# Kernel optimization log

Measured on AMD Instinct MI355X. Metric: run time of the kernel, lower is better.

## Reference

```python
import jax, jax.numpy as jnp
import numpy as np

N_GRAPHS = 100
NODES_PER_GRAPH = 1000
N = N_GRAPHS * NODES_PER_GRAPH
DEG = 16
E = N * DEG
IN_FEATS = 64
HIDDEN = 128
READOUT_DIM = HIDDEN // 2
SLOPE = 0.01
EPS = 1e-5


def leaky(x):
    return jnp.where(x >= 0, x, SLOPE * x)


def _kaiming(k, shape):
    # torch kaiming_uniform_, fan_in mode, leaky_relu gain
    fan_in = shape[0]
    gain = np.sqrt(2.0 / (1.0 + SLOPE ** 2))
    bound = gain * np.sqrt(3.0 / fan_in)
    return jax.random.uniform(k, shape, jnp.float32, -bound, bound)


def setup_inputs() -> dict:
    key = jax.random.key(0)
    ks = jax.random.split(key, 16)
    node_feats = jax.random.normal(ks[0], (N, IN_FEATS), jnp.float32)
    # within-graph random edges (batched graph of equal-sized components)
    src_local = jax.random.randint(ks[1], (E,), 0, NODES_PER_GRAPH)
    dst_local = jax.random.randint(ks[2], (E,), 0, NODES_PER_GRAPH)
    edge_graph = jnp.repeat(jnp.arange(N_GRAPHS, dtype=jnp.int32), E // N_GRAPHS)
    src = (edge_graph * NODES_PER_GRAPH + src_local).astype(jnp.int32)
    dst = (edge_graph * NODES_PER_GRAPH + dst_local).astype(jnp.int32)
    edge_weights = jax.random.uniform(ks[3], (E,), jnp.float32)
    node_graph = jnp.repeat(jnp.arange(N_GRAPHS, dtype=jnp.int32), NODES_PER_GRAPH)
    return {
        "node_feats": node_feats,
        "edge_weights": edge_weights,
        "W1": _kaiming(ks[4], (IN_FEATS, HIDDEN)),
        "W2": _kaiming(ks[5], (HIDDEN, HIDDEN)),
        "gn1_alpha": jnp.ones((HIDDEN,), jnp.float32),
        "gn1_gamma": jnp.ones((HIDDEN,), jnp.float32),
        "gn1_beta": jnp.zeros((HIDDEN,), jnp.float32),
        "gn2_alpha": jnp.ones((HIDDEN,), jnp.float32),
        "gn2_gamma": jnp.ones((HIDDEN,), jnp.float32),
        "gn2_beta": jnp.zeros((HIDDEN,), jnp.float32),
        "r1_w1": _kaiming(ks[6], (HIDDEN, HIDDEN)),
        "r1_b1": jnp.zeros((HIDDEN,), jnp.float32),
        "r1_w2": _kaiming(ks[7], (HIDDEN, READOUT_DIM)),
        "r1_b2": jnp.zeros((READOUT_DIM,), jnp.float32),
        "r2_w1": _kaiming(ks[8], (HIDDEN, HIDDEN)),
        "r2_b1": jnp.zeros((HIDDEN,), jnp.float32),
        "r2_w2": _kaiming(ks[9], (HIDDEN, READOUT_DIM)),
        "r2_b2": jnp.zeros((READOUT_DIM,), jnp.float32),
        "src": src,
        "dst": dst,
        "node_graph": node_graph,
    }


def _graph_conv(x, W, src, dst, ew, out_isqrt, in_isqrt):
    # DGL GraphConv norm='both', no bias: D_in^{-1/2} A_w D_out^{-1/2} X W
    h = (x * out_isqrt[:, None]) @ W                 # [N, out]
    m = h[src] * ew[:, None]                         # [E, out] gather + edge weight
    agg = jax.ops.segment_sum(m, dst, num_segments=N)  # scatter-add
    return agg * in_isqrt[:, None]


def _graph_norm(x, alpha, gamma, beta, node_graph, inv_cnt):
    mean = jax.ops.segment_sum(x, node_graph, num_segments=N_GRAPHS) * inv_cnt
    sub = x - alpha * mean[node_graph]
    var = jax.ops.segment_sum(sub * sub, node_graph, num_segments=N_GRAPHS) * inv_cnt
    return gamma * sub / jnp.sqrt(var[node_graph] + EPS) + beta


def _readout(x, w1, b1, w2, b2, node_graph, inv_cnt):
    # deep-sets style universal readout: rho(mean(phi(h_v)))
    h = leaky(x @ w1 + b1)
    pooled = jax.ops.segment_sum(h, node_graph, num_segments=N_GRAPHS) * inv_cnt
    return leaky(pooled @ w2 + b2)


def reference(node_feats, edge_weights, W1, W2,
              gn1_alpha, gn1_gamma, gn1_beta,
              gn2_alpha, gn2_gamma, gn2_beta,
              r1_w1, r1_b1, r1_w2, r1_b2,
              r2_w1, r2_b1, r2_w2, r2_b2,
              src, dst, node_graph):
    ones_e = jnp.ones((E,), jnp.float32)
    out_deg = jnp.clip(jax.ops.segment_sum(ones_e, src, num_segments=N), 1.0)
    in_deg = jnp.clip(jax.ops.segment_sum(ones_e, dst, num_segments=N), 1.0)
    out_isqrt = jax.lax.rsqrt(out_deg)
    in_isqrt = jax.lax.rsqrt(in_deg)
    inv_cnt = 1.0 / NODES_PER_GRAPH

    h = _graph_conv(node_feats, W1, src, dst, edge_weights, out_isqrt, in_isqrt)
    h = leaky(_graph_norm(h, gn1_alpha, gn1_gamma, gn1_beta, node_graph, inv_cnt))
    # dropout is identity in eval mode
    r1 = _readout(h, r1_w1, r1_b1, r1_w2, r1_b2, node_graph, inv_cnt)
    m1 = jax.ops.segment_sum(h, node_graph, num_segments=N_GRAPHS) * inv_cnt

    h = _graph_conv(h, W2, src, dst, edge_weights, out_isqrt, in_isqrt)
    h = leaky(_graph_norm(h, gn2_alpha, gn2_gamma, gn2_beta, node_graph, inv_cnt))
    r2 = _readout(h, r2_w1, r2_b1, r2_w2, r2_b2, node_graph, inv_cnt)
    m2 = jax.ops.segment_sum(h, node_graph, num_segments=N_GRAPHS) * inv_cnt

    readout = jnp.concatenate([r1, m1, r2, m2], axis=1)  # [G, 2*H + 2*H/2] = [100, 384]
    return leaky(readout)
```

## Files before the change

### kernel.cpp

```cpp
#include <hip/hip_runtime.h>
#include <cstddef>
#include <cstdint>

#define NG   100
#define NPG  1000
#define NN   (NG * NPG)
#define NE   (NN * 16)
#define EPG  (NE / NG)
#define CSRG 40000
#define MINREC 20
#define FIN  64
#define HID  128
#define RD   64
#define SLOPE 0.01f
#define EPSV  1e-5f
#define NSTRIP 250
#define GSN   40

using short8 = __attribute__((ext_vector_type(8))) short;
using f32x4  = __attribute__((ext_vector_type(4))) float;
typedef unsigned short u16;

__device__ __forceinline__ float leaky(float x) { return x >= 0.f ? x : SLOPE * x; }

__device__ __forceinline__ u16 f2bf(float f) {
  union { float f; unsigned u; } v; v.f = f;
  return (u16)((v.u + 0x7fffu + ((v.u >> 16) & 1u)) >> 16);
}
__device__ __forceinline__ float bf2f(u16 u) {
  union { unsigned u; float f; } v; v.u = ((unsigned)u) << 16;
  return v.f;
}

__device__ __forceinline__ bool swz(int b, int per_g, int& g, int& part) {
  const int xcd = b & 7;
  const int slot = b >> 3;
  g = xcd + 8 * (slot / per_g);
  part = slot % per_g;
  return g < NG;
}

__global__ __launch_bounds__(256) void wt_k(const float* __restrict__ W1,
                                            const float* __restrict__ W2,
                                            const float* __restrict__ R1,
                                            const float* __restrict__ R2,
                                            u16* __restrict__ Wt1,
                                            u16* __restrict__ Wt2,
                                            u16* __restrict__ Rt1,
                                            u16* __restrict__ Rt2) {
  const int idx = blockIdx.x * 256 + threadIdx.x;
  if (idx < FIN * HID) {
    const int n = idx >> 6, k = idx & 63;
    Wt1[idx] = f2bf(W1[k * HID + n]);
  } else {
    const int j = idx - FIN * HID;
    const int m = j >> 14, r = j & 16383;
    const int n = r >> 7, k = r & 127;
    const float* s = (m == 0) ? W2 : (m == 1) ? R1 : R2;
    u16* d = (m == 0) ? Wt2 : (m == 1) ? Rt1 : Rt2;
    d[r] = f2bf(s[k * HID + n]);
  }
}

__global__ __launch_bounds__(1024) void build_k(const int* __restrict__ src,
                                                const int* __restrict__ dst,
                                                const float* __restrict__ ew,
                                                int* __restrict__ cin_,
                                                int* __restrict__ cout_,
                                                int* __restrict__ offs,
                                                unsigned* __restrict__ csr) {
  __shared__ int hin[NPG];
  __shared__ int hout[NPG];
  __shared__ int cur[NPG];
  __shared__ int wtot[16];
  int g, part;
  if (!swz(blockIdx.x, 1, g, part)) return;
  const int t = threadIdx.x;
  const int lane = t & 63, wave = t >> 6;
  const int nb = g * NPG, eb = g * EPG;
  if (t < NPG) { hin[t] = 0; hout[t] = 0; }
  __syncthreads();
  for (int e = t; e < EPG; e += 4096) {
    int s4[4], d4[4];
#pragma unroll
    for (int k = 0; k < 4; ++k) {
      const int ee = e + k * 1024;
      if (ee < EPG) { s4[k] = src[eb + ee]; d4[k] = dst[eb + ee]; }
      else d4[k] = -1;
    }
#pragma unroll
    for (int k = 0; k < 4; ++k)
      if (d4[k] >= 0) {
        atomicAdd(&hout[s4[k] - nb], 1);
        atomicAdd(&hin[d4[k] - nb], 1);
      }
  }
  __syncthreads();
  int v[4], vr[4];
  int loc = 0;
#pragma unroll
  for (int k = 0; k < 4; ++k) {
    const int idx = t * 4 + k;
    v[k] = (idx < NPG) ? hin[idx] : 0;
    const int c4 = (v[k] + 3) & ~3;
    vr[k] = (idx < NPG) ? ((c4 > MINREC) ? c4 : MINREC) : 0;
    loc += vr[k];
  }
  int incl = loc;
#pragma unroll
  for (int d = 1; d < 64; d <<= 1) {
    const int x = __shfl_up(incl, d);
    if (lane >= d) incl += x;
  }
  if (lane == 63) wtot[wave] = incl;
  if (t < NPG) { cin_[nb + t] = hin[t]; cout_[nb + t] = hout[t]; }
  __syncthreads();
  int wexc = 0;
  for (int i = 0; i < wave; ++i) wexc += wtot[i];
  int run = g * CSRG + wexc + (incl - loc);
#pragma unroll
  for (int k = 0; k < 4; ++k) {
    const int idx = t * 4 + k;
    if (idx < NPG) {
      offs[nb + idx] = run;
      cur[idx] = run;
      for (int z = v[k]; z < vr[k]; ++z) csr[run + z] = 0;
      run += vr[k];
    }
  }
  __syncthreads();
  for (int e = t; e < EPG; e += 4096) {
    int s4[4], d4[4]; float w4[4];
#pragma unroll
    for (int k = 0; k < 4; ++k) {
      const int ee = e + k * 1024;
      if (ee < EPG) { s4[k] = src[eb + ee]; d4[k] = dst[eb + ee]; w4[k] = ew[eb + ee]; }
      else d4[k] = -1;
    }
#pragma unroll
    for (int k = 0; k < 4; ++k)
      if (d4[k] >= 0) {
        const int pos = atomicAdd(&cur[d4[k] - nb], 1);
        csr[pos] = ((unsigned)(s4[k] - nb) << 16) | (unsigned)f2bf(w4[k]);
      }
  }
}

__global__ __launch_bounds__(256) void gemm1_k(const float* __restrict__ X,
                                               const u16* __restrict__ Wt,
                                               const int* __restrict__ cout_,
                                               u16* __restrict__ Y) {
  __shared__ u16 Xl[64 * FIN];
  __shared__ u16 Wl[HID * FIN];
  const int tid = threadIdx.x;
  const int wave = tid >> 6, lane = tid & 63, l15 = lane & 15, quad = lane >> 4;
  int g, part;
  if (!swz(blockIdx.x, 4, g, part)) return;
  const int base = g * NPG + part * NSTRIP;
  const int kq = tid & 15;
  const int srow = tid >> 4;

  for (int i = tid; i < HID * (FIN / 8); i += 256) {
    const int n = i >> 3, c = i & 7;
    const short8 w = *(const short8*)(Wt + n * FIN + c * 8);
    *(short8*)&Wl[n * FIN + ((c ^ (n & 7)) << 3)] = w;
  }
  float4 xpre[4];
#pragma unroll
  for (int it = 0; it < 4; ++it) {
    const int rowi = srow + it * 16;
    xpre[it] = (rowi < NSTRIP) ? *(const float4*)(X + (size_t)(base + rowi) * FIN + kq * 4)
                               : make_float4(0.f, 0.f, 0.f, 0.f);
  }
  for (int pass = 0; pass < 4; ++pass) {
    __syncthreads();
#pragma unroll
    for (int it = 0; it < 4; ++it) {
      const int r = srow + it * 16;
      ushort4 u = make_ushort4(f2bf(xpre[it].x), f2bf(xpre[it].y),
                               f2bf(xpre[it].z), f2bf(xpre[it].w));
      const int c = kq >> 1, half = kq & 1;
      *(ushort4*)&Xl[r * FIN + (((c ^ (r & 7)) << 3) | (half << 2))] = u;
    }
    __syncthreads();
    if (pass < 3) {
#pragma unroll
      for (int it = 0; it < 4; ++it) {
        const int rowi = (pass + 1) * 64 + srow + it * 16;
        xpre[it] = (rowi < NSTRIP) ? *(const float4*)(X + (size_t)(base + rowi) * FIN + kq * 4)
                                   : make_float4(0.f, 0.f, 0.f, 0.f);
      }
    }
    short8 a[2];
    const int arow = wave * 16 + l15;
#pragma unroll
    for (int kt = 0; kt < 2; ++kt)
      a[kt] = *(const short8*)&Xl[arow * FIN + (((kt * 4 + quad) ^ (l15 & 7)) << 3)];
    float sc[4];
    int rows[4];
#pragma unroll
    for (int r = 0; r < 4; ++r) {
      rows[r] = pass * 64 + wave * 16 + quad * 4 + r;
      sc[r] = (rows[r] < NSTRIP) ? rsqrtf(fmaxf((float)cout_[base + rows[r]], 1.0f)) : 0.f;
    }
#pragma unroll
    for (int ct = 0; ct < 8; ++ct) {
      f32x4 acc = {0.f, 0.f, 0.f, 0.f};
      const int brow = ct * 16 + l15;
#pragma unroll
      for (int kt = 0; kt < 2; ++kt) {
        const short8 b = *(const short8*)&Wl[brow * FIN + (((kt * 4 + quad) ^ (l15 & 7)) << 3)];
        acc = __builtin_amdgcn_mfma_f32_16x16x32_bf16(a[kt], b, acc, 0, 0, 0);
      }
      const int n = ct * 16 + l15;
#pragma unroll
      for (int r = 0; r < 4; ++r)
        if (rows[r] < NSTRIP) Y[(size_t)(base + rows[r]) * HID + n] = f2bf(acc[r] * sc[r]);
    }
  }
}

__device__ __forceinline__ void norm_affine(const float* sx, const float* sq,
                                            const float* alpha, const float* gamma,
                                            const float* beta, int g, int c8,
                                            float* Av, float* Bv) {
  const float inv = 1.0f / NPG;
#pragma unroll
  for (int j = 0; j < 8; ++j) {
    const int f = c8 * 8 + j;
    const float mean = sx[g * HID + f] * inv;
    const float ex2 = sq[g * HID + f] * inv;
    const float am = alpha[f] * mean;
    const float var = fmaxf(ex2 - 2.0f * am * mean + am * am, 0.0f);
    const float A = gamma[f] * rsqrtf(var + EPSV);
    Av[j] = A;
    Bv[j] = beta[f] - A * am;
  }
}

__global__ __launch_bounds__(256) void gemm_norm_k(const u16* __restrict__ Xb,
                                                   const u16* __restrict__ Wt,
                                                   const float* __restrict__ sx,
                                                   const float* __restrict__ sq,
                                                   const float* __restrict__ alpha,
                                                   const float* __restrict__ gamma,
                                                   const float* __restrict__ beta,
                                                   const int* __restrict__ cout_,
                                                   u16* __restrict__ Y) {
  __shared__ u16 Xl[64 * HID];
  __shared__ u16 Wl[HID * HID];
  const int tid = threadIdx.x;
  const int wave = tid >> 6, lane = tid & 63, l15 = lane & 15, quad = lane >> 4;
  int g, part;
  if (!swz(blockIdx.x, 4, g, part)) return;
  const int base = g * NPG + part * NSTRIP;
  const int c8 = tid & 15;
  const int srow = tid >> 4;

  for (int i = tid; i < HID * (HID / 8); i += 256) {
    const int n = i >> 4, c = i & 15;
    const short8 w = *(const short8*)(Wt + n * HID + c * 8);
    *(short8*)&Wl[n * HID + ((c ^ (n & 15)) << 3)] = w;
  }
  float Av[8], Bv[8];
  norm_affine(sx, sq, alpha, gamma, beta, g, c8, Av, Bv);
  const short8 z8 = {0, 0, 0, 0, 0, 0, 0, 0};
  short8 xpre[4];
#pragma unroll
  for (int it = 0; it < 4; ++it) {
    const int rowi = srow + it * 16;
    xpre[it] = (rowi < NSTRIP) ? *(const short8*)(Xb + (size_t)(base + rowi) * HID + c8 * 8) : z8;
  }
  for (int pass = 0; pass < 4; ++pass) {
    __syncthreads();
#pragma unroll
    for (int it = 0; it < 4; ++it) {
      const int r = srow + it * 16;
      const int rowi = pass * 64 + r;
      short8 o = z8;
      if (rowi < NSTRIP) {
#pragma unroll
        for (int j = 0; j < 8; ++j)
          o[j] = (short)f2bf(leaky(fmaf(Av[j], bf2f((u16)xpre[it][j]), Bv[j])));
      }
      *(short8*)&Xl[r * HID + ((c8 ^ (r & 15)) << 3)] = o;
    }
    __syncthreads();
    if (pass < 3) {
#pragma unroll
      for (int it = 0; it < 4; ++it) {
        const int rowi = (pass + 1) * 64 + srow + it * 16;
        xpre[it] = (rowi < NSTRIP) ? *(const short8*)(Xb + (size_t)(base + rowi) * HID + c8 * 8) : z8;
      }
    }
    short8 a[4];
    const int arow = wave * 16 + l15;
#pragma unroll
    for (int kt = 0; kt < 4; ++kt)
      a[kt] = *(const short8*)&Xl[arow * HID + (((kt * 4 + quad) ^ l15) << 3)];
    float sc[4];
    int rows[4];
#pragma unroll
    for (int r = 0; r < 4; ++r) {
      rows[r] = pass * 64 + wave * 16 + quad * 4 + r;
      sc[r] = (rows[r] < NSTRIP) ? rsqrtf(fmaxf((float)cout_[base + rows[r]], 1.0f)) : 0.f;
    }
#pragma unroll
    for (int ct = 0; ct < 8; ++ct) {
      f32x4 acc = {0.f, 0.f, 0.f, 0.f};
      const int brow = ct * 16 + l15;
#pragma unroll
      for (int kt = 0; kt < 4; ++kt) {
        const short8 b = *(const short8*)&Wl[brow * HID + (((kt * 4 + quad) ^ l15) << 3)];
        acc = __builtin_amdgcn_mfma_f32_16x16x32_bf16(a[kt], b, acc, 0, 0, 0);
      }
      const int n = ct * 16 + l15;
#pragma unroll
      for (int r = 0; r < 4; ++r)
        if (rows[r] < NSTRIP) Y[(size_t)(base + rows[r]) * HID + n] = f2bf(acc[r] * sc[r]);
    }
  }
}

struct RedT { float red[16][HID]; float hred[16][HID]; };
union ShT { u16 Xl[64 * HID]; RedT r; };

__global__ __launch_bounds__(256) void phi_pool_k(const u16* __restrict__ Xb,
                                                  const float* __restrict__ sx,
                                                  const float* __restrict__ sq,
                                                  const float* __restrict__ alpha,
                                                  const float* __restrict__ gamma,
                                                  const float* __restrict__ beta,
                                                  const u16* __restrict__ Wt,
                                                  const float* __restrict__ b1,
                                                  float* __restrict__ phi_sum,
                                                  float* __restrict__ h_sum) {
  __shared__ ShT sh;
  __shared__ u16 Wl[HID * HID];
  const int tid = threadIdx.x;
  const int wave = tid >> 6, lane = tid & 63, l15 = lane & 15, quad = lane >> 4;
  int g, part;
  if (!swz(blockIdx.x, 4, g, part)) return;
  const int base = g * NPG + part * NSTRIP;
  const int c8 = tid & 15;
  const int srow = tid >> 4;

  for (int i = tid; i < HID * (HID / 8); i += 256) {
    const int n = i >> 4, c = i & 15;
    const short8 w = *(const short8*)(Wt + n * HID + c * 8);
    *(short8*)&Wl[n * HID + ((c ^ (n & 15)) << 3)] = w;
  }
  float Av[8], Bv[8];
  norm_affine(sx, sq, alpha, gamma, beta, g, c8, Av, Bv);
  float bcol[8];
#pragma unroll
  for (int ct = 0; ct < 8; ++ct) bcol[ct] = b1[ct * 16 + l15];

  float pooled[8] = {0.f, 0.f, 0.f, 0.f, 0.f, 0.f, 0.f, 0.f};
  float hp[8] = {0.f, 0.f, 0.f, 0.f, 0.f, 0.f, 0.f, 0.f};
  const short8 z8 = {0, 0, 0, 0, 0, 0, 0, 0};
  short8 xpre[4];
#pragma unroll
  for (int it = 0; it < 4; ++it) {
    const int rowi = srow + it * 16;
    xpre[it] = (rowi < NSTRIP) ? *(const short8*)(Xb + (size_t)(base + rowi) * HID + c8 * 8) : z8;
  }
  for (int pass = 0; pass < 4; ++pass) {
    __syncthreads();
#pragma unroll
    for (int it = 0; it < 4; ++it) {
      const int r = srow + it * 16;
      const int rowi = pass * 64 + r;
      short8 o = z8;
      if (rowi < NSTRIP) {
#pragma unroll
        for (int j = 0; j < 8; ++j) {
          const float xn = leaky(fmaf(Av[j], bf2f((u16)xpre[it][j]), Bv[j]));
          hp[j] += xn;
          o[j] = (short)f2bf(xn);
        }
      }
      *(short8*)&sh.Xl[r * HID + ((c8 ^ (r & 15)) << 3)] = o;
    }
    __syncthreads();
    if (pass < 3) {
#pragma unroll
      for (int it = 0; it < 4; ++it) {
        const int rowi = (pass + 1) * 64 + srow + it * 16;
        xpre[it] = (rowi < NSTRIP) ? *(const short8*)(Xb + (size_t)(base + rowi) * HID + c8 * 8) : z8;
      }
    }
    short8 a[4];
    const int arow = wave * 16 + l15;
#pragma unroll
    for (int kt = 0; kt < 4; ++kt)
      a[kt] = *(const short8*)&sh.Xl[arow * HID + (((kt * 4 + quad) ^ l15) << 3)];
#pragma unroll
    for (int ct = 0; ct < 8; ++ct) {
      f32x4 acc = {0.f, 0.f, 0.f, 0.f};
      const int brow = ct * 16 + l15;
#pragma unroll
      for (int kt = 0; kt < 4; ++kt) {
        const short8 b = *(const short8*)&Wl[brow * HID + (((kt * 4 + quad) ^ l15) << 3)];
        acc = __builtin_amdgcn_mfma_f32_16x16x32_bf16(a[kt], b, acc, 0, 0, 0);
      }
#pragma unroll
      for (int r = 0; r < 4; ++r) {
        const int rowi = pass * 64 + wave * 16 + quad * 4 + r;
        if (rowi < NSTRIP) pooled[ct] += leaky(acc[r] + bcol[ct]);
      }
    }
  }
  __syncthreads();
  const int qi = wave * 4 + quad;
#pragma unroll
  for (int ct = 0; ct < 8; ++ct) sh.r.red[qi][ct * 16 + l15] = pooled[ct];
#pragma unroll
  for (int j = 0; j < 8; ++j) sh.r.hred[tid >> 4][(tid & 15) * 8 + j] = hp[j];
  __syncthreads();
  if (tid < HID) {
    float s = 0.f;
#pragma unroll
    for (int q = 0; q < 16; ++q) s += sh.r.red[q][tid];
    unsafeAtomicAdd(&phi_sum[g * HID + tid], s);
  } else {
    const int t = tid - HID;
    float s = 0.f;
#pragma unroll
    for (int rr = 0; rr < 16; ++rr) s += sh.r.hred[rr][t];
    unsafeAtomicAdd(&h_sum[g * HID + t], s);
  }
}

__global__ __launch_bounds__(256) void gather_k(const u16* __restrict__ H,
                                                const unsigned* __restrict__ csr,
                                                const int* __restrict__ offs,
                                                const int* __restrict__ cin_,
                                                u16* __restrict__ AGG,
                                                float* __restrict__ sx,
                                                float* __restrict__ sq) {
  __shared__ float redx[4][HID];
  __shared__ float redq[4][HID];
  const int wave = threadIdx.x >> 6;
  const int lane = threadIdx.x & 63;
  int g, part;
  if (!swz(blockIdx.x, 25, g, part)) return;
  const int nb = g * NPG;
  const int base = nb + part * GSN;
  const int loff = lane * 2;
  const u16* __restrict__ Hg = H + (size_t)nb * HID;

  float sxa = 0.f, sxb = 0.f, sqa = 0.f, sqb = 0.f;
  for (int it = 0; it < 3; ++it) {
    const int nc = (it < 2) ? 4 : 2;
    int nn[4], off[4], cnt[4], c4p[4];
    float isq[4];
    const uint4* p[4];
#pragma unroll
    for (int c = 0; c < 4; ++c) {
      const int j = it * 4 + c;
      const int node = base + wave + ((j < 10) ? j : 0) * 4;
      nn[c] = node;
      const int nu = __builtin_amdgcn_readfirstlane(node);
      off[c] = __builtin_amdgcn_readfirstlane(offs[nu]);
      cnt[c] = (c < nc) ? __builtin_amdgcn_readfirstlane(cin_[nu]) : 0;
      const int cr = (cnt[c] + 3) & ~3;
      c4p[c] = ((cr > MINREC) ? cr : MINREC) >> 2;
      isq[c] = rsqrtf(fmaxf((float)cnt[c], 1.0f));
      p[c] = (const uint4*)__builtin_assume_aligned(csr + off[c], 16);
    }
    float ax[4] = {0.f, 0.f, 0.f, 0.f};
    float ay[4] = {0.f, 0.f, 0.f, 0.f};
#pragma unroll
    for (int t = 0; t < 5; ++t) {
      uint4 r[4];
      unsigned u[4][4];
#pragma unroll
      for (int c = 0; c < 4; ++c)
        if (c < nc) {
          r[c] = p[c][t];
          u[c][0] = *(const unsigned*)(Hg + (size_t)(r[c].x >> 16) * HID + loff);
          u[c][1] = *(const unsigned*)(Hg + (size_t)(r[c].y >> 16) * HID + loff);
          u[c][2] = *(const unsigned*)(Hg + (size_t)(r[c].z >> 16) * HID + loff);
          u[c][3] = *(const unsigned*)(Hg + (size_t)(r[c].w >> 16) * HID + loff);
        }
#pragma unroll
      for (int c = 0; c < 4; ++c)
        if (c < nc) {
          const float w0 = bf2f((u16)(r[c].x & 0xffffu));
          const float w1 = bf2f((u16)(r[c].y & 0xffffu));
          const float w2 = bf2f((u16)(r[c].z & 0xffffu));
          const float w3 = bf2f((u16)(r[c].w & 0xffffu));
          ax[c] = fmaf(w0, __uint_as_float(u[c][0] << 16), ax[c]);
          ay[c] = fmaf(w0, __uint_as_float(u[c][0] & 0xffff0000u), ay[c]);
          ax[c] = fmaf(w1, __uint_as_float(u[c][1] << 16), ax[c]);
          ay[c] = fmaf(w1, __uint_as_float(u[c][1] & 0xffff0000u), ay[c]);
          ax[c] = fmaf(w2, __uint_as_float(u[c][2] << 16), ax[c]);
          ay[c] = fmaf(w2, __uint_as_float(u[c][2] & 0xffff0000u), ay[c]);
          ax[c] = fmaf(w3, __uint_as_float(u[c][3] << 16), ax[c]);
          ay[c] = fmaf(w3, __uint_as_float(u[c][3] & 0xffff0000u), ay[c]);
        }
    }
#pragma unroll
    for (int c = 0; c < 4; ++c) {
      for (int t = 5; t < c4p[c]; ++t) {
        const uint4 r = p[c][t];
        const unsigned u0 = *(const unsigned*)(Hg + (size_t)(r.x >> 16) * HID + loff);
        const unsigned u1 = *(const unsigned*)(Hg + (size_t)(r.y >> 16) * HID + loff);
        const unsigned u2 = *(const unsigned*)(Hg + (size_t)(r.z >> 16) * HID + loff);
        const unsigned u3 = *(const unsigned*)(Hg + (size_t)(r.w >> 16) * HID + loff);
        const float w0 = bf2f((u16)(r.x & 0xffffu));
        const float w1 = bf2f((u16)(r.y & 0xffffu));
        const float w2 = bf2f((u16)(r.z & 0xffffu));
        const float w3 = bf2f((u16)(r.w & 0xffffu));
        ax[c] = fmaf(w0, __uint_as_float(u0 << 16), ax[c]);
        ay[c] = fmaf(w0, __uint_as_float(u0 & 0xffff0000u), ay[c]);
        ax[c] = fmaf(w1, __uint_as_float(u1 << 16), ax[c]);
        ay[c] = fmaf(w1, __uint_as_float(u1 & 0xffff0000u), ay[c]);
        ax[c] = fmaf(w2, __uint_as_float(u2 << 16), ax[c]);
        ay[c] = fmaf(w2, __uint_as_float(u2 & 0xffff0000u), ay[c]);
        ax[c] = fmaf(w3, __uint_as_float(u3 << 16), ax[c]);
        ay[c] = fmaf(w3, __uint_as_float(u3 & 0xffff0000u), ay[c]);
      }
    }
#pragma unroll
    for (int c = 0; c < 4; ++c)
      if (c < nc) {
        const float rx = ax[c] * isq[c];
        const float ry = ay[c] * isq[c];
        *(unsigned*)(AGG + (size_t)nn[c] * HID + loff) =
            (unsigned)f2bf(rx) | ((unsigned)f2bf(ry) << 16);
        sxa += rx; sxb += ry;
        sqa += rx * rx; sqb += ry * ry;
      }
  }
  redx[wave][loff] = sxa; redx[wave][loff + 1] = sxb;
  redq[wave][loff] = sqa; redq[wave][loff + 1] = sqb;
  __syncthreads();
  const int tid = threadIdx.x;
  if (tid < HID) {
    unsafeAtomicAdd(&sx[g * HID + tid],
                    redx[0][tid] + redx[1][tid] + redx[2][tid] + redx[3][tid]);
  } else {
    const int t = tid - HID;
    unsafeAtomicAdd(&sq[g * HID + t],
                    redq[0][t] + redq[1][t] + redq[2][t] + redq[3][t]);
  }
}

__global__ __launch_bounds__(64) void finalize_k(const float* __restrict__ phi_sum,
                                                 const float* __restrict__ h_sum,
                                                 const float* __restrict__ w2,
                                                 const float* __restrict__ b2,
                                                 float* __restrict__ out,
                                                 int roff, int moff) {
  const int g = blockIdx.x;
  const int j = threadIdx.x;
  float acc = b2[j];
#pragma unroll 8
  for (int k = 0; k < HID; ++k)
    acc += (phi_sum[g * HID + k] * (1.0f / NPG)) * w2[k * RD + j];
  const float r = leaky(acc);
  out[g * 384 + roff + j] = leaky(r);
  out[g * 384 + moff + j] = leaky(h_sum[g * HID + j] * (1.0f / NPG));
  out[g * 384 + moff + 64 + j] = leaky(h_sum[g * HID + 64 + j] * (1.0f / NPG));
}

extern "C" void kernel_launch(void* const* d_in, const int* in_sizes, int n_in,
                              void* d_out, int out_size, void* d_ws, size_t ws_size,
                              hipStream_t stream) {
  const float* node_feats = (const float*)d_in[0];
  const float* ew   = (const float*)d_in[1];
  const float* W1   = (const float*)d_in[2];
  const float* W2   = (const float*)d_in[3];
  const float* g1a  = (const float*)d_in[4];
  const float* g1g  = (const float*)d_in[5];
  const float* g1b  = (const float*)d_in[6];
  const float* g2a  = (const float*)d_in[7];
  const float* g2g  = (const float*)d_in[8];
  const float* g2b  = (const float*)d_in[9];
  const float* r1w1 = (const float*)d_in[10];
  const float* r1b1 = (const float*)d_in[11];
  const float* r1w2 = (const float*)d_in[12];
  const float* r1b2 = (const float*)d_in[13];
  const float* r2w1 = (const float*)d_in[14];
  const float* r2b1 = (const float*)d_in[15];
  const float* r2w2 = (const float*)d_in[16];
  const float* r2b2 = (const float*)d_in[17];
  const int* src = (const int*)d_in[18];
  const int* dst = (const int*)d_in[19];
  float* out = (float*)d_out;

  char* wsb = (char*)d_ws;
  float* ps1     = (float*)wsb;
  float* hs1     = ps1 + NG * HID;
  float* ps2     = hs1 + NG * HID;
  float* hs2     = ps2 + NG * HID;
  float* sx1     = hs2 + NG * HID;
  float* sq1     = sx1 + NG * HID;
  float* sx2     = sq1 + NG * HID;
  float* sq2     = sx2 + NG * HID;
  int*   cin     = (int*)(sq2 + NG * HID);
  int*   cout_   = cin + NN;
  int*   offs    = cout_ + NN;
  unsigned* csr  = (unsigned*)(offs + NN);
  u16*   Wt1     = (u16*)(csr + (size_t)NG * CSRG);
  u16*   Wt2     = Wt1 + HID * FIN;
  u16*   Rt1     = Wt2 + HID * HID;
  u16*   Rt2     = Rt1 + HID * HID;
  u16*   bufA    = Rt2 + HID * HID;
  u16*   bufB    = bufA + (size_t)NN * HID;

  hipMemsetAsync(d_ws, 0, (size_t)(8 * NG * HID) * sizeof(float), stream);

  wt_k<<<(FIN * HID + 3 * HID * HID) / 256, 256, 0, stream>>>(
      W1, W2, r1w1, r2w1, Wt1, Wt2, Rt1, Rt2);
  build_k<<<8 * 13, 1024, 0, stream>>>(src, dst, ew, cin, cout_, offs, csr);

  const int gemm_grid = 8 * 4 * 13;
  const int gather_grid = 8 * 25 * 13;

  gemm1_k<<<gemm_grid, 256, 0, stream>>>(node_feats, Wt1, cout_, bufA);
  gather_k<<<gather_grid, 256, 0, stream>>>(bufA, csr, offs, cin, bufB, sx1, sq1);
  phi_pool_k<<<gemm_grid, 256, 0, stream>>>(bufB, sx1, sq1, g1a, g1g, g1b,
                                            Rt1, r1b1, ps1, hs1);
  finalize_k<<<NG, 64, 0, stream>>>(ps1, hs1, r1w2, r1b2, out, 0, 64);

  gemm_norm_k<<<gemm_grid, 256, 0, stream>>>(bufB, Wt2, sx1, sq1, g1a, g1g, g1b,
                                             cout_, bufA);
  gather_k<<<gather_grid, 256, 0, stream>>>(bufA, csr, offs, cin, bufB, sx2, sq2);
  phi_pool_k<<<gemm_grid, 256, 0, stream>>>(bufB, sx2, sq2, g2a, g2g, g2b,
                                            Rt2, r2b1, ps2, hs2);
  finalize_k<<<NG, 64, 0, stream>>>(ps2, hs2, r2w2, r2b2, out, 192, 256);
}
```

Measured before the change: 294.2 us.

## Fuse all per-graph stages into one persistent 1024-thread block per graph

```diff
diff --git a/kernel.cpp b/kernel.cpp
--- a/kernel.cpp
+++ b/kernel.cpp
@@ -14,8 +14,6 @@
 #define RD   64
 #define SLOPE 0.01f
 #define EPSV  1e-5f
-#define NSTRIP 250
-#define GSN   40
 
 using short8 = __attribute__((ext_vector_type(8))) short;
 using f32x4  = __attribute__((ext_vector_type(4))) float;
@@ -30,14 +28,6 @@
 __device__ __forceinline__ float bf2f(u16 u) {
   union { unsigned u; float f; } v; v.u = ((unsigned)u) << 16;
   return v.f;
-}
-
-__device__ __forceinline__ bool swz(int b, int per_g, int& g, int& part) {
-  const int xcd = b & 7;
-  const int slot = b >> 3;
-  g = xcd + 8 * (slot / per_g);
-  part = slot % per_g;
-  return g < NG;
 }
 
 __global__ __launch_bounds__(256) void wt_k(const float* __restrict__ W1,
@@ -62,449 +52,73 @@
   }
 }
 
-__global__ __launch_bounds__(1024) void build_k(const int* __restrict__ src,
-                                                const int* __restrict__ dst,
-                                                const float* __restrict__ ew,
-                                                int* __restrict__ cin_,
-                                                int* __restrict__ cout_,
-                                                int* __restrict__ offs,
-                                                unsigned* __restrict__ csr) {
-  __shared__ int hin[NPG];
-  __shared__ int hout[NPG];
-  __shared__ int cur[NPG];
-  __shared__ int wtot[16];
-  int g, part;
-  if (!swz(blockIdx.x, 1, g, part)) return;
+struct BldU { int cur[NPG]; int wtot[16]; };
+struct RedU { float redx[16][HID]; float redq[16][HID]; };
+struct PhiU { float red4[4][HID]; float hred[16][HID]; };
+union MegaU { BldU b; u16 Xl[64 * HID]; RedU r; PhiU p; };
+
+__device__ __forceinline__ void gather_stage(const u16* __restrict__ Hg,
+                                             const unsigned* __restrict__ csr,
+                                             u16* __restrict__ AGGg, MegaU* u,
+                                             const int* s_hin, const int* s_offs,
+                                             float* s_sx, float* s_sq) {
   const int t = threadIdx.x;
-  const int lane = t & 63, wave = t >> 6;
-  const int nb = g * NPG, eb = g * EPG;
-  if (t < NPG) { hin[t] = 0; hout[t] = 0; }
-  __syncthreads();
-  for (int e = t; e < EPG; e += 4096) {
-    int s4[4], d4[4];
-#pragma unroll
-    for (int k = 0; k < 4; ++k) {
-      const int ee = e + k * 1024;
-      if (ee < EPG) { s4[k] = src[eb + ee]; d4[k] = dst[eb + ee]; }
-      else d4[k] = -1;
-    }
-#pragma unroll
-    for (int k = 0; k < 4; ++k)
-      if (d4[k] >= 0) {
-        atomicAdd(&hout[s4[k] - nb], 1);
-        atomicAdd(&hin[d4[k] - nb], 1);
-      }
-  }
-  __syncthreads();
-  int v[4], vr[4];
-  int loc = 0;
-#pragma unroll
-  for (int k = 0; k < 4; ++k) {
-    const int idx = t * 4 + k;
-    v[k] = (idx < NPG) ? hin[idx] : 0;
-    const int c4 = (v[k] + 3) & ~3;
-    vr[k] = (idx < NPG) ? ((c4 > MINREC) ? c4 : MINREC) : 0;
-    loc += vr[k];
-  }
-  int incl = loc;
-#pragma unroll
-  for (int d = 1; d < 64; d <<= 1) {
-    const int x = __shfl_up(incl, d);
-    if (lane >= d) incl += x;
-  }
-  if (lane == 63) wtot[wave] = incl;
-  if (t < NPG) { cin_[nb + t] = hin[t]; cout_[nb + t] = hout[t]; }
-  __syncthreads();
-  int wexc = 0;
-  for (int i = 0; i < wave; ++i) wexc += wtot[i];
-  int run = g * CSRG + wexc + (incl - loc);
-#pragma unroll
-  for (int k = 0; k < 4; ++k) {
-    const int idx = t * 4 + k;
-    if (idx < NPG) {
-      offs[nb + idx] = run;
-      cur[idx] = run;
-      for (int z = v[k]; z < vr[k]; ++z) csr[run + z] = 0;
-      run += vr[k];
-    }
-  }
-  __syncthreads();
-  for (int e = t; e < EPG; e += 4096) {
-    int s4[4], d4[4]; float w4[4];
-#pragma unroll
-    for (int k = 0; k < 4; ++k) {
-      const int ee = e + k * 1024;
-      if (ee < EPG) { s4[k] = src[eb + ee]; d4[k] = dst[eb + ee]; w4[k] = ew[eb + ee]; }
-      else d4[k] = -1;
-    }
-#pragma unroll
-    for (int k = 0; k < 4; ++k)
-      if (d4[k] >= 0) {
-        const int pos = atomicAdd(&cur[d4[k] - nb], 1);
-        csr[pos] = ((unsigned)(s4[k] - nb) << 16) | (unsigned)f2bf(w4[k]);
-      }
-  }
-}
-
-__global__ __launch_bounds__(256) void gemm1_k(const float* __restrict__ X,
-                                               const u16* __restrict__ Wt,
-                                               const int* __restrict__ cout_,
-                                               u16* __restrict__ Y) {
-  __shared__ u16 Xl[64 * FIN];
-  __shared__ u16 Wl[HID * FIN];
-  const int tid = threadIdx.x;
-  const int wave = tid >> 6, lane = tid & 63, l15 = lane & 15, quad = lane >> 4;
-  int g, part;
-  if (!swz(blockIdx.x, 4, g, part)) return;
-  const int base = g * NPG + part * NSTRIP;
-  const int kq = tid & 15;
-  const int srow = tid >> 4;
-
-  for (int i = tid; i < HID * (FIN / 8); i += 256) {
-    const int n = i >> 3, c = i & 7;
-    const short8 w = *(const short8*)(Wt + n * FIN + c * 8);
-    *(short8*)&Wl[n * FIN + ((c ^ (n & 7)) << 3)] = w;
-  }
-  float4 xpre[4];
-#pragma unroll
-  for (int it = 0; it < 4; ++it) {
-    const int rowi = srow + it * 16;
-    xpre[it] = (rowi < NSTRIP) ? *(const float4*)(X + (size_t)(base + rowi) * FIN + kq * 4)
-                               : make_float4(0.f, 0.f, 0.f, 0.f);
-  }
-  for (int pass = 0; pass < 4; ++pass) {
-    __syncthreads();
-#pragma unroll
-    for (int it = 0; it < 4; ++it) {
-      const int r = srow + it * 16;
-      ushort4 u = make_ushort4(f2bf(xpre[it].x), f2bf(xpre[it].y),
-                               f2bf(xpre[it].z), f2bf(xpre[it].w));
-      const int c = kq >> 1, half = kq & 1;
-      *(ushort4*)&Xl[r * FIN + (((c ^ (r & 7)) << 3) | (half << 2))] = u;
-    }
-    __syncthreads();
-    if (pass < 3) {
-#pragma unroll
-      for (int it = 0; it < 4; ++it) {
-        const int rowi = (pass + 1) * 64 + srow + it * 16;
-        xpre[it] = (rowi < NSTRIP) ? *(const float4*)(X + (size_t)(base + rowi) * FIN + kq * 4)
-                                   : make_float4(0.f, 0.f, 0.f, 0.f);
-      }
-    }
-    short8 a[2];
-    const int arow = wave * 16 + l15;
-#pragma unroll
-    for (int kt = 0; kt < 2; ++kt)
-      a[kt] = *(const short8*)&Xl[arow * FIN + (((kt * 4 + quad) ^ (l15 & 7)) << 3)];
-    float sc[4];
-    int rows[4];
-#pragma unroll
-    for (int r = 0; r < 4; ++r) {
-      rows[r] = pass * 64 + wave * 16 + quad * 4 + r;
-      sc[r] = (rows[r] < NSTRIP) ? rsqrtf(fmaxf((float)cout_[base + rows[r]], 1.0f)) : 0.f;
-    }
-#pragma unroll
-    for (int ct = 0; ct < 8; ++ct) {
-      f32x4 acc = {0.f, 0.f, 0.f, 0.f};
-      const int brow = ct * 16 + l15;
-#pragma unroll
-      for (int kt = 0; kt < 2; ++kt) {
-        const short8 b = *(const short8*)&Wl[brow * FIN + (((kt * 4 + quad) ^ (l15 & 7)) << 3)];
-        acc = __builtin_amdgcn_mfma_f32_16x16x32_bf16(a[kt], b, acc, 0, 0, 0);
-      }
-      const int n = ct * 16 + l15;
-#pragma unroll
-      for (int r = 0; r < 4; ++r)
-        if (rows[r] < NSTRIP) Y[(size_t)(base + rows[r]) * HID + n] = f2bf(acc[r] * sc[r]);
-    }
-  }
-}
-
-__device__ __forceinline__ void norm_affine(const float* sx, const float* sq,
-                                            const float* alpha, const float* gamma,
-                                            const float* beta, int g, int c8,
-                                            float* Av, float* Bv) {
-  const float inv = 1.0f / NPG;
-#pragma unroll
-  for (int j = 0; j < 8; ++j) {
-    const int f = c8 * 8 + j;
-    const float mean = sx[g * HID + f] * inv;
-    const float ex2 = sq[g * HID + f] * inv;
-    const float am = alpha[f] * mean;
-    const float var = fmaxf(ex2 - 2.0f * am * mean + am * am, 0.0f);
-    const float A = gamma[f] * rsqrtf(var + EPSV);
-    Av[j] = A;
-    Bv[j] = beta[f] - A * am;
-  }
-}
-
-__global__ __launch_bounds__(256) void gemm_norm_k(const u16* __restrict__ Xb,
-                                                   const u16* __restrict__ Wt,
-                                                   const float* __restrict__ sx,
-                                                   const float* __restrict__ sq,
-                                                   const float* __restrict__ alpha,
-                                                   const float* __restrict__ gamma,
-                                                   const float* __restrict__ beta,
-                                                   const int* __restrict__ cout_,
-                                                   u16* __restrict__ Y) {
-  __shared__ u16 Xl[64 * HID];
-  __shared__ u16 Wl[HID * HID];
-  const int tid = threadIdx.x;
-  const int wave = tid >> 6, lane = tid & 63, l15 = lane & 15, quad = lane >> 4;
-  int g, part;
-  if (!swz(blockIdx.x, 4, g, part)) return;
-  const int base = g * NPG + part * NSTRIP;
-  const int c8 = tid & 15;
-  const int srow = tid >> 4;
-
-  for (int i = tid; i < HID * (HID / 8); i += 256) {
-    const int n = i >> 4, c = i & 15;
-    const short8 w = *(const short8*)(Wt + n * HID + c * 8);
-    *(short8*)&Wl[n * HID + ((c ^ (n & 15)) << 3)] = w;
-  }
-  float Av[8], Bv[8];
-  norm_affine(sx, sq, alpha, gamma, beta, g, c8, Av, Bv);
-  const short8 z8 = {0, 0, 0, 0, 0, 0, 0, 0};
-  short8 xpre[4];
-#pragma unroll
-  for (int it = 0; it < 4; ++it) {
-    const int rowi = srow + it * 16;
-    xpre[it] = (rowi < NSTRIP) ? *(const short8*)(Xb + (size_t)(base + rowi) * HID + c8 * 8) : z8;
-  }
-  for (int pass = 0; pass < 4; ++pass) {
-    __syncthreads();
-#pragma unroll
-    for (int it = 0; it < 4; ++it) {
-      const int r = srow + it * 16;
-      const int rowi = pass * 64 + r;
-      short8 o = z8;
-      if (rowi < NSTRIP) {
-#pragma unroll
-        for (int j = 0; j < 8; ++j)
-          o[j] = (short)f2bf(leaky(fmaf(Av[j], bf2f((u16)xpre[it][j]), Bv[j])));
-      }
-      *(short8*)&Xl[r * HID + ((c8 ^ (r & 15)) << 3)] = o;
-    }
-    __syncthreads();
-    if (pass < 3) {
-#pragma unroll
-      for (int it = 0; it < 4; ++it) {
-        const int rowi = (pass + 1) * 64 + srow + it * 16;
-        xpre[it] = (rowi < NSTRIP) ? *(const short8*)(Xb + (size_t)(base + rowi) * HID + c8 * 8) : z8;
-      }
-    }
-    short8 a[4];
-    const int arow = wave * 16 + l15;
-#pragma unroll
-    for (int kt = 0; kt < 4; ++kt)
-      a[kt] = *(const short8*)&Xl[arow * HID + (((kt * 4 + quad) ^ l15) << 3)];
-    float sc[4];
-    int rows[4];
-#pragma unroll
-    for (int r = 0; r < 4; ++r) {
-      rows[r] = pass * 64 + wave * 16 + quad * 4 + r;
-      sc[r] = (rows[r] < NSTRIP) ? rsqrtf(fmaxf((float)cout_[base + rows[r]], 1.0f)) : 0.f;
-    }
-#pragma unroll
-    for (int ct = 0; ct < 8; ++ct) {
-      f32x4 acc = {0.f, 0.f, 0.f, 0.f};
-      const int brow = ct * 16 + l15;
-#pragma unroll
-      for (int kt = 0; kt < 4; ++kt) {
-        const short8 b = *(const short8*)&Wl[brow * HID + (((kt * 4 + quad) ^ l15) << 3)];
-        acc = __builtin_amdgcn_mfma_f32_16x16x32_bf16(a[kt], b, acc, 0, 0, 0);
-      }
-      const int n = ct * 16 + l15;
-#pragma unroll
-      for (int r = 0; r < 4; ++r)
-        if (rows[r] < NSTRIP) Y[(size_t)(base + rows[r]) * HID + n] = f2bf(acc[r] * sc[r]);
-    }
-  }
-}
-
-struct RedT { float red[16][HID]; float hred[16][HID]; };
-union ShT { u16 Xl[64 * HID]; RedT r; };
-
-__global__ __launch_bounds__(256) void phi_pool_k(const u16* __restrict__ Xb,
-                                                  const float* __restrict__ sx,
-                                                  const float* __restrict__ sq,
-                                                  const float* __restrict__ alpha,
-                                                  const float* __restrict__ gamma,
-                                                  const float* __restrict__ beta,
-                                                  const u16* __restrict__ Wt,
-                                                  const float* __restrict__ b1,
-                                                  float* __restrict__ phi_sum,
-                                                  float* __restrict__ h_sum) {
-  __shared__ ShT sh;
-  __shared__ u16 Wl[HID * HID];
-  const int tid = threadIdx.x;
-  const int wave = tid >> 6, lane = tid & 63, l15 = lane & 15, quad = lane >> 4;
-  int g, part;
-  if (!swz(blockIdx.x, 4, g, part)) return;
-  const int base = g * NPG + part * NSTRIP;
-  const int c8 = tid & 15;
-  const int srow = tid >> 4;
-
-  for (int i = tid; i < HID * (HID / 8); i += 256) {
-    const int n = i >> 4, c = i & 15;
-    const short8 w = *(const short8*)(Wt + n * HID + c * 8);
-    *(short8*)&Wl[n * HID + ((c ^ (n & 15)) << 3)] = w;
-  }
-  float Av[8], Bv[8];
-  norm_affine(sx, sq, alpha, gamma, beta, g, c8, Av, Bv);
-  float bcol[8];
-#pragma unroll
-  for (int ct = 0; ct < 8; ++ct) bcol[ct] = b1[ct * 16 + l15];
-
-  float pooled[8] = {0.f, 0.f, 0.f, 0.f, 0.f, 0.f, 0.f, 0.f};
-  float hp[8] = {0.f, 0.f, 0.f, 0.f, 0.f, 0.f, 0.f, 0.f};
-  const short8 z8 = {0, 0, 0, 0, 0, 0, 0, 0};
-  short8 xpre[4];
-#pragma unroll
-  for (int it = 0; it < 4; ++it) {
-    const int rowi = srow + it * 16;
-    xpre[it] = (rowi < NSTRIP) ? *(const short8*)(Xb + (size_t)(base + rowi) * HID + c8 * 8) : z8;
-  }
-  for (int pass = 0; pass < 4; ++pass) {
-    __syncthreads();
-#pragma unroll
-    for (int it = 0; it < 4; ++it) {
-      const int r = srow + it * 16;
-      const int rowi = pass * 64 + r;
-      short8 o = z8;
-      if (rowi < NSTRIP) {
-#pragma unroll
-        for (int j = 0; j < 8; ++j) {
-          const float xn = leaky(fmaf(Av[j], bf2f((u16)xpre[it][j]), Bv[j]));
-          hp[j] += xn;
-          o[j] = (short)f2bf(xn);
-        }
-      }
-      *(short8*)&sh.Xl[r * HID + ((c8 ^ (r & 15)) << 3)] = o;
-    }
-    __syncthreads();
-    if (pass < 3) {
-#pragma unroll
-      for (int it = 0; it < 4; ++it) {
-        const int rowi = (pass + 1) * 64 + srow + it * 16;
-        xpre[it] = (rowi < NSTRIP) ? *(const short8*)(Xb + (size_t)(base + rowi) * HID + c8 * 8) : z8;
-      }
-    }
-    short8 a[4];
-    const int arow = wave * 16 + l15;
-#pragma unroll
-    for (int kt = 0; kt < 4; ++kt)
-      a[kt] = *(const short8*)&sh.Xl[arow * HID + (((kt * 4 + quad) ^ l15) << 3)];
-#pragma unroll
-    for (int ct = 0; ct < 8; ++ct) {
-      f32x4 acc = {0.f, 0.f, 0.f, 0.f};
-      const int brow = ct * 16 + l15;
-#pragma unroll
-      for (int kt = 0; kt < 4; ++kt) {
-        const short8 b = *(const short8*)&Wl[brow * HID + (((kt * 4 + quad) ^ l15) << 3)];
-        acc = __builtin_amdgcn_mfma_f32_16x16x32_bf16(a[kt], b, acc, 0, 0, 0);
-      }
-#pragma unroll
-      for (int r = 0; r < 4; ++r) {
-        const int rowi = pass * 64 + wave * 16 + quad * 4 + r;
-        if (rowi < NSTRIP) pooled[ct] += leaky(acc[r] + bcol[ct]);
-      }
-    }
-  }
-  __syncthreads();
-  const int qi = wave * 4 + quad;
-#pragma unroll
-  for (int ct = 0; ct < 8; ++ct) sh.r.red[qi][ct * 16 + l15] = pooled[ct];
-#pragma unroll
-  for (int j = 0; j < 8; ++j) sh.r.hred[tid >> 4][(tid & 15) * 8 + j] = hp[j];
-  __syncthreads();
-  if (tid < HID) {
-    float s = 0.f;
-#pragma unroll
-    for (int q = 0; q < 16; ++q) s += sh.r.red[q][tid];
-    unsafeAtomicAdd(&phi_sum[g * HID + tid], s);
-  } else {
-    const int t = tid - HID;
-    float s = 0.f;
-#pragma unroll
-    for (int rr = 0; rr < 16; ++rr) s += sh.r.hred[rr][t];
-    unsafeAtomicAdd(&h_sum[g * HID + t], s);
-  }
-}
-
-__global__ __launch_bounds__(256) void gather_k(const u16* __restrict__ H,
-                                                const unsigned* __restrict__ csr,
-                                                const int* __restrict__ offs,
-                                                const int* __restrict__ cin_,
-                                                u16* __restrict__ AGG,
-                                                float* __restrict__ sx,
-                                                float* __restrict__ sq) {
-  __shared__ float redx[4][HID];
-  __shared__ float redq[4][HID];
-  const int wave = threadIdx.x >> 6;
-  const int lane = threadIdx.x & 63;
-  int g, part;
-  if (!swz(blockIdx.x, 25, g, part)) return;
-  const int nb = g * NPG;
-  const int base = nb + part * GSN;
+  const int wave = t >> 6, lane = t & 63;
   const int loff = lane * 2;
-  const u16* __restrict__ Hg = H + (size_t)nb * HID;
-
   float sxa = 0.f, sxb = 0.f, sqa = 0.f, sqb = 0.f;
-  for (int it = 0; it < 3; ++it) {
-    const int nc = (it < 2) ? 4 : 2;
-    int nn[4], off[4], cnt[4], c4p[4];
+  for (int it = 0; it < 16; ++it) {
+    int nn[4], cnt[4], c4p[4], val[4];
     float isq[4];
     const uint4* p[4];
 #pragma unroll
     for (int c = 0; c < 4; ++c) {
-      const int j = it * 4 + c;
-      const int node = base + wave + ((j < 10) ? j : 0) * 4;
-      nn[c] = node;
-      const int nu = __builtin_amdgcn_readfirstlane(node);
-      off[c] = __builtin_amdgcn_readfirstlane(offs[nu]);
-      cnt[c] = (c < nc) ? __builtin_amdgcn_readfirstlane(cin_[nu]) : 0;
+      const int idx = wave + 16 * (it * 4 + c);
+      val[c] = (idx < NPG);
+      const int idc = val[c] ? idx : 0;
+      nn[c] = idc;
+      const int off = __builtin_amdgcn_readfirstlane(s_offs[idc]);
+      cnt[c] = val[c] ? __builtin_amdgcn_readfirstlane(s_hin[idc]) : 0;
       const int cr = (cnt[c] + 3) & ~3;
       c4p[c] = ((cr > MINREC) ? cr : MINREC) >> 2;
       isq[c] = rsqrtf(fmaxf((float)cnt[c], 1.0f));
-      p[c] = (const uint4*)__builtin_assume_aligned(csr + off[c], 16);
+      p[c] = (const uint4*)__builtin_assume_aligned(csr + off, 16);
     }
     float ax[4] = {0.f, 0.f, 0.f, 0.f};
     float ay[4] = {0.f, 0.f, 0.f, 0.f};
 #pragma unroll
-    for (int t = 0; t < 5; ++t) {
+    for (int tt = 0; tt < 5; ++tt) {
       uint4 r[4];
-      unsigned u[4][4];
+      unsigned uu[4][4];
 #pragma unroll
       for (int c = 0; c < 4; ++c)
-        if (c < nc) {
-          r[c] = p[c][t];
-          u[c][0] = *(const unsigned*)(Hg + (size_t)(r[c].x >> 16) * HID + loff);
-          u[c][1] = *(const unsigned*)(Hg + (size_t)(r[c].y >> 16) * HID + loff);
-          u[c][2] = *(const unsigned*)(Hg + (size_t)(r[c].z >> 16) * HID + loff);
-          u[c][3] = *(const unsigned*)(Hg + (size_t)(r[c].w >> 16) * HID + loff);
+        if (val[c]) {
+          r[c] = p[c][tt];
+          uu[c][0] = *(const unsigned*)(Hg + (size_t)(r[c].x >> 16) * HID + loff);
+          uu[c][1] = *(const unsigned*)(Hg + (size_t)(r[c].y >> 16) * HID + loff);
+          uu[c][2] = *(const unsigned*)(Hg + (size_t)(r[c].z >> 16) * HID + loff);
+          uu[c][3] = *(const unsigned*)(Hg + (size_t)(r[c].w >> 16) * HID + loff);
         }
 #pragma unroll
       for (int c = 0; c < 4; ++c)
-        if (c < nc) {
+        if (val[c]) {
           const float w0 = bf2f((u16)(r[c].x & 0xffffu));
           const float w1 = bf2f((u16)(r[c].y & 0xffffu));
           const float w2 = bf2f((u16)(r[c].z & 0xffffu));
           const float w3 = bf2f((u16)(r[c].w & 0xffffu));
-          ax[c] = fmaf(w0, __uint_as_float(u[c][0] << 16), ax[c]);
-          ay[c] = fmaf(w0, __uint_as_float(u[c][0] & 0xffff0000u), ay[c]);
-          ax[c] = fmaf(w1, __uint_as_float(u[c][1] << 16), ax[c]);
-          ay[c] = fmaf(w1, __uint_as_float(u[c][1] & 0xffff0000u), ay[c]);
-          ax[c] = fmaf(w2, __uint_as_float(u[c][2] << 16), ax[c]);
-          ay[c] = fmaf(w2, __uint_as_float(u[c][2] & 0xffff0000u), ay[c]);
-          ax[c] = fmaf(w3, __uint_as_float(u[c][3] << 16), ax[c]);
-          ay[c] = fmaf(w3, __uint_as_float(u[c][3] & 0xffff0000u), ay[c]);
+          ax[c] = fmaf(w0, __uint_as_float(uu[c][0] << 16), ax[c]);
+          ay[c] = fmaf(w0, __uint_as_float(uu[c][0] & 0xffff0000u), ay[c]);
+          ax[c] = fmaf(w1, __uint_as_float(uu[c][1] << 16), ax[c]);
+          ay[c] = fmaf(w1, __uint_as_float(uu[c][1] & 0xffff0000u), ay[c]);
+          ax[c] = fmaf(w2, __uint_as_float(uu[c][2] << 16), ax[c]);
+          ay[c] = fmaf(w2, __uint_as_float(uu[c][2] & 0xffff0000u), ay[c]);
+          ax[c] = fmaf(w3, __uint_as_float(uu[c][3] << 16), ax[c]);
+          ay[c] = fmaf(w3, __uint_as_float(uu[c][3] & 0xffff0000u), ay[c]);
         }
     }
 #pragma unroll
     for (int c = 0; c < 4; ++c) {
-      for (int t = 5; t < c4p[c]; ++t) {
-        const uint4 r = p[c][t];
+      for (int tt = 5; tt < c4p[c]; ++tt) {
+        const uint4 r = p[c][tt];
         const unsigned u0 = *(const unsigned*)(Hg + (size_t)(r.x >> 16) * HID + loff);
         const unsigned u1 = *(const unsigned*)(Hg + (size_t)(r.y >> 16) * HID + loff);
         const unsigned u2 = *(const unsigned*)(Hg + (size_t)(r.z >> 16) * HID + loff);
@@ -525,45 +139,363 @@
     }
 #pragma unroll
     for (int c = 0; c < 4; ++c)
-      if (c < nc) {
+      if (val[c]) {
         const float rx = ax[c] * isq[c];
         const float ry = ay[c] * isq[c];
-        *(unsigned*)(AGG + (size_t)nn[c] * HID + loff) =
+        *(unsigned*)(AGGg + (size_t)nn[c] * HID + loff) =
             (unsigned)f2bf(rx) | ((unsigned)f2bf(ry) << 16);
         sxa += rx; sxb += ry;
         sqa += rx * rx; sqb += ry * ry;
       }
   }
-  redx[wave][loff] = sxa; redx[wave][loff + 1] = sxb;
-  redq[wave][loff] = sqa; redq[wave][loff + 1] = sqb;
-  __syncthreads();
-  const int tid = threadIdx.x;
-  if (tid < HID) {
-    unsafeAtomicAdd(&sx[g * HID + tid],
-                    redx[0][tid] + redx[1][tid] + redx[2][tid] + redx[3][tid]);
-  } else {
-    const int t = tid - HID;
-    unsafeAtomicAdd(&sq[g * HID + t],
-                    redq[0][t] + redq[1][t] + redq[2][t] + redq[3][t]);
-  }
-}
-
-__global__ __launch_bounds__(64) void finalize_k(const float* __restrict__ phi_sum,
-                                                 const float* __restrict__ h_sum,
-                                                 const float* __restrict__ w2,
-                                                 const float* __restrict__ b2,
-                                                 float* __restrict__ out,
-                                                 int roff, int moff) {
+  u->r.redx[wave][loff] = sxa; u->r.redx[wave][loff + 1] = sxb;
+  u->r.redq[wave][loff] = sqa; u->r.redq[wave][loff + 1] = sqb;
+  __syncthreads();
+  if (t < HID) {
+    float s = 0.f;
+#pragma unroll
+    for (int w = 0; w < 16; ++w) s += u->r.redx[w][t];
+    s_sx[t] = s;
+  } else if (t < 2 * HID) {
+    const int c = t - HID;
+    float s = 0.f;
+#pragma unroll
+    for (int w = 0; w < 16; ++w) s += u->r.redq[w][c];
+    s_sq[c] = s;
+  }
+  __syncthreads();
+}
+
+template <bool DO_GEMM>
+__device__ __forceinline__ void phi_stage(const u16* __restrict__ Xin,
+                                          u16* __restrict__ Yout,
+                                          const u16* __restrict__ WtG,
+                                          const u16* __restrict__ RtG,
+                                          const float* __restrict__ bias1,
+                                          const float* __restrict__ alpha,
+                                          const float* __restrict__ gamma,
+                                          const float* __restrict__ beta,
+                                          MegaU* u, u16* sW, u16* sR,
+                                          const int* s_hout,
+                                          const float* s_sx, const float* s_sq,
+                                          float* ps_out, float* hs_out) {
+  const int t = threadIdx.x;
+  const int wave = t >> 6, lane = t & 63, l15 = lane & 15, quad = lane >> 4;
+  const int rg = wave >> 2, cg = wave & 3;
+  const int c8 = t & 15, srow = t >> 4;
+
+  for (int i = t; i < HID * (HID / 8); i += 1024) {
+    const int n = i >> 4, c = i & 15;
+    if (DO_GEMM) {
+      const short8 w = *(const short8*)(WtG + n * HID + c * 8);
+      *(short8*)&sW[n * HID + ((c ^ (n & 15)) << 3)] = w;
+    }
+    const short8 w2 = *(const short8*)(RtG + n * HID + c * 8);
+    *(short8*)&sR[n * HID + ((c ^ (n & 15)) << 3)] = w2;
+  }
+  const float inv = 1.0f / NPG;
+  float Av[8], Bv[8];
+#pragma unroll
+  for (int j = 0; j < 8; ++j) {
+    const int f = c8 * 8 + j;
+    const float mean = s_sx[f] * inv;
+    const float ex2 = s_sq[f] * inv;
+    const float am = alpha[f] * mean;
+    const float var = fmaxf(ex2 - 2.0f * am * mean + am * am, 0.0f);
+    const float A = gamma[f] * rsqrtf(var + EPSV);
+    Av[j] = A;
+    Bv[j] = beta[f] - A * am;
+  }
+  float bcol[2];
+#pragma unroll
+  for (int q2 = 0; q2 < 2; ++q2) bcol[q2] = bias1[(cg * 2 + q2) * 16 + l15];
+
+  float pooled[2] = {0.f, 0.f};
+  float hp[8] = {0.f, 0.f, 0.f, 0.f, 0.f, 0.f, 0.f, 0.f};
+  const short8 z8 = {0, 0, 0, 0, 0, 0, 0, 0};
+  short8 xpre = (srow < NPG) ? *(const short8*)(Xin + (size_t)srow * HID + c8 * 8) : z8;
+
+  for (int pass = 0; pass < 16; ++pass) {
+    __syncthreads();
+    {
+      const int rowi = pass * 64 + srow;
+      short8 o = z8;
+      if (rowi < NPG) {
+#pragma unroll
+        for (int j = 0; j < 8; ++j) {
+          const float xn = leaky(fmaf(Av[j], bf2f((u16)xpre[j]), Bv[j]));
+          hp[j] += xn;
+          o[j] = (short)f2bf(xn);
+        }
+      }
+      *(short8*)&u->Xl[srow * HID + ((c8 ^ (srow & 15)) << 3)] = o;
+    }
+    __syncthreads();
+    if (pass < 15) {
+      const int rowi = (pass + 1) * 64 + srow;
+      xpre = (rowi < NPG) ? *(const short8*)(Xin + (size_t)rowi * HID + c8 * 8) : z8;
+    }
+    short8 a[4];
+    const int arow = rg * 16 + l15;
+#pragma unroll
+    for (int kt = 0; kt < 4; ++kt)
+      a[kt] = *(const short8*)&u->Xl[arow * HID + (((kt * 4 + quad) ^ l15) << 3)];
+    int rows[4];
+    float sc[4];
+#pragma unroll
+    for (int r = 0; r < 4; ++r) {
+      rows[r] = pass * 64 + rg * 16 + quad * 4 + r;
+      sc[r] = (rows[r] < NPG) ? rsqrtf(fmaxf((float)s_hout[rows[r]], 1.0f)) : 0.f;
+    }
+#pragma unroll
+    for (int q2 = 0; q2 < 2; ++q2) {
+      const int ct = cg * 2 + q2;
+      const int brow = ct * 16 + l15;
+      if (DO_GEMM) {
+        f32x4 accW = {0.f, 0.f, 0.f, 0.f};
+#pragma unroll
+        for (int kt = 0; kt < 4; ++kt) {
+          const short8 b = *(const short8*)&sW[brow * HID + (((kt * 4 + quad) ^ l15) << 3)];
+          accW = __builtin_amdgcn_mfma_f32_16x16x32_bf16(a[kt], b, accW, 0, 0, 0);
+        }
+#pragma unroll
+        for (int r = 0; r < 4; ++r)
+          if (rows[r] < NPG)
+            Yout[(size_t)rows[r] * HID + ct * 16 + l15] = f2bf(accW[r] * sc[r]);
+      }
+      f32x4 accR = {0.f, 0.f, 0.f, 0.f};
+#pragma unroll
+      for (int kt = 0; kt < 4; ++kt) {
+        const short8 b = *(const short8*)&sR[brow * HID + (((kt * 4 + quad) ^ l15) << 3)];
+        accR = __builtin_amdgcn_mfma_f32_16x16x32_bf16(a[kt], b, accR, 0, 0, 0);
+      }
+#pragma unroll
+      for (int r = 0; r < 4; ++r)
+        if (rows[r] < NPG) pooled[q2] += leaky(accR[r] + bcol[q2]);
+    }
+  }
+  __syncthreads();
+#pragma unroll
+  for (int q2 = 0; q2 < 2; ++q2) {
+    pooled[q2] += __shfl_xor(pooled[q2], 16);
+    pooled[q2] += __shfl_xor(pooled[q2], 32);
+  }
+  if (quad == 0) {
+#pragma unroll
+    for (int q2 = 0; q2 < 2; ++q2)
+      u->p.red4[rg][(cg * 2 + q2) * 16 + l15] = pooled[q2];
+  }
+#pragma unroll
+  for (int j = 0; j < 8; ++j) {
+    hp[j] += __shfl_xor(hp[j], 16);
+    hp[j] += __shfl_xor(hp[j], 32);
+  }
+  if (lane < 16) {
+#pragma unroll
+    for (int j = 0; j < 8; ++j) u->p.hred[wave][(lane & 15) * 8 + j] = hp[j];
+  }
+  __syncthreads();
+  if (t < HID) {
+    float s = 0.f;
+#pragma unroll
+    for (int k = 0; k < 4; ++k) s += u->p.red4[k][t];
+    ps_out[t] = s;
+  } else if (t < 2 * HID) {
+    const int c = t - HID;
+    float s = 0.f;
+#pragma unroll
+    for (int w = 0; w < 16; ++w) s += u->p.hred[w][c];
+    hs_out[c] = s;
+  }
+  __syncthreads();
+}
+
+__global__ __launch_bounds__(1024, 1) void mega_k(
+    const float* __restrict__ X0, const float* __restrict__ ew,
+    const int* __restrict__ src, const int* __restrict__ dst,
+    const u16* __restrict__ Wt1, const u16* __restrict__ Wt2,
+    const u16* __restrict__ Rt1, const u16* __restrict__ Rt2,
+    const float* __restrict__ g1a, const float* __restrict__ g1g,
+    const float* __restrict__ g1b, const float* __restrict__ g2a,
+    const float* __restrict__ g2g, const float* __restrict__ g2b,
+    const float* __restrict__ r1b1, const float* __restrict__ r1w2,
+    const float* __restrict__ r1b2, const float* __restrict__ r2b1,
+    const float* __restrict__ r2w2, const float* __restrict__ r2b2,
+    unsigned* __restrict__ csr, u16* __restrict__ bufA, u16* __restrict__ bufB,
+    float* __restrict__ out) {
+  __shared__ u16 sW[HID * HID];
+  __shared__ u16 sR[HID * HID];
+  __shared__ int s_hin[NPG];
+  __shared__ int s_hout[NPG];
+  __shared__ int s_offs[NPG];
+  __shared__ float s_sx[HID], s_sq[HID];
+  __shared__ float s_ps[2][HID], s_hs[2][HID];
+  __shared__ MegaU u;
+
   const int g = blockIdx.x;
-  const int j = threadIdx.x;
-  float acc = b2[j];
+  const int t = threadIdx.x;
+  const int wave = t >> 6, lane = t & 63, l15 = lane & 15, quad = lane >> 4;
+  const int nb = g * NPG, eb = g * EPG;
+
+  if (t < NPG) { s_hin[t] = 0; s_hout[t] = 0; }
+  __syncthreads();
+  for (int e = t; e < EPG; e += 4096) {
+    int s4[4], d4[4];
+#pragma unroll
+    for (int k = 0; k < 4; ++k) {
+      const int ee = e + k * 1024;
+      if (ee < EPG) { s4[k] = src[eb + ee]; d4[k] = dst[eb + ee]; }
+      else d4[k] = -1;
+    }
+#pragma unroll
+    for (int k = 0; k < 4; ++k)
+      if (d4[k] >= 0) {
+        atomicAdd(&s_hout[s4[k] - nb], 1);
+        atomicAdd(&s_hin[d4[k] - nb], 1);
+      }
+  }
+  __syncthreads();
+  {
+    int v[4], vr[4];
+    int loc = 0;
+#pragma unroll
+    for (int k = 0; k < 4; ++k) {
+      const int idx = t * 4 + k;
+      v[k] = (idx < NPG) ? s_hin[idx] : 0;
+      const int c4 = (v[k] + 3) & ~3;
+      vr[k] = (idx < NPG) ? ((c4 > MINREC) ? c4 : MINREC) : 0;
+      loc += vr[k];
+    }
+    int incl = loc;
+#pragma unroll
+    for (int d = 1; d < 64; d <<= 1) {
+      const int x = __shfl_up(incl, d);
+      if (lane >= d) incl += x;
+    }
+    if (lane == 63) u.b.wtot[wave] = incl;
+    __syncthreads();
+    int wexc = 0;
+    for (int i = 0; i < wave; ++i) wexc += u.b.wtot[i];
+    int run = g * CSRG + wexc + (incl - loc);
+#pragma unroll
+    for (int k = 0; k < 4; ++k) {
+      const int idx = t * 4 + k;
+      if (idx < NPG) {
+        s_offs[idx] = run;
+        u.b.cur[idx] = run;
+        for (int z = v[k]; z < vr[k]; ++z) csr[run + z] = 0;
+        run += vr[k];
+      }
+    }
+  }
+  __syncthreads();
+  for (int e = t; e < EPG; e += 4096) {
+    int s4[4], d4[4];
+    float w4[4];
+#pragma unroll
+    for (int k = 0; k < 4; ++k) {
+      const int ee = e + k * 1024;
+      if (ee < EPG) { s4[k] = src[eb + ee]; d4[k] = dst[eb + ee]; w4[k] = ew[eb + ee]; }
+      else d4[k] = -1;
+    }
+#pragma unroll
+    for (int k = 0; k < 4; ++k)
+      if (d4[k] >= 0) {
+        const int pos = atomicAdd(&u.b.cur[d4[k] - nb], 1);
+        csr[pos] = ((unsigned)(s4[k] - nb) << 16) | (unsigned)f2bf(w4[k]);
+      }
+  }
+  __syncthreads();
+
+  {
+    const int n = t >> 3, c = t & 7;
+    const short8 w = *(const short8*)(Wt1 + n * FIN + c * 8);
+    *(short8*)&sW[n * FIN + ((c ^ (n & 7)) << 3)] = w;
+  }
+  const int kq = t & 15, srow = t >> 4;
+  const int rg = wave >> 2, cg = wave & 3;
+  {
+    float4 xpre = (srow < NPG)
+        ? *(const float4*)(X0 + (size_t)(nb + srow) * FIN + kq * 4)
+        : make_float4(0.f, 0.f, 0.f, 0.f);
+    for (int pass = 0; pass < 16; ++pass) {
+      __syncthreads();
+      {
+        ushort4 uu = make_ushort4(f2bf(xpre.x), f2bf(xpre.y), f2bf(xpre.z), f2bf(xpre.w));
+        const int cc = kq >> 1, half = kq & 1;
+        *(ushort4*)&u.Xl[srow * FIN + (((cc ^ (srow & 7)) << 3) | (half << 2))] = uu;
+      }
+      __syncthreads();
+      if (pass < 15) {
+        const int rowi = (pass + 1) * 64 + srow;
+        xpre = (rowi < NPG)
+            ? *(const float4*)(X0 + (size_t)(nb + rowi) * FIN + kq * 4)
+            : make_float4(0.f, 0.f, 0.f, 0.f);
+      }
+      short8 a[2];
+      const int arow = rg * 16 + l15;
+#pragma unroll
+      for (int kt = 0; kt < 2; ++kt)
+        a[kt] = *(const short8*)&u.Xl[arow * FIN + (((kt * 4 + quad) ^ (l15 & 7)) << 3)];
+      int rows[4];
+      float sc[4];
+#pragma unroll
+      for (int r = 0; r < 4; ++r) {
+        rows[r] = pass * 64 + rg * 16 + quad * 4 + r;
+        sc[r] = (rows[r] < NPG) ? rsqrtf(fmaxf((float)s_hout[rows[r]], 1.0f)) : 0.f;
+      }
+#pragma unroll
+      for (int q2 = 0; q2 < 2; ++q2) {
+        const int ct = cg * 2 + q2;
+        f32x4 acc = {0.f, 0.f, 0.f, 0.f};
+        const int brow = ct * 16 + l15;
+#pragma unroll
+        for (int kt = 0; kt < 2; ++kt) {
+          const short8 b = *(const short8*)&sW[brow * FIN + (((kt * 4 + quad) ^ (l15 & 7)) << 3)];
+          acc = __builtin_amdgcn_mfma_f32_16x16x32_bf16(a[kt], b, acc, 0, 0, 0);
+        }
+        const int n2 = ct * 16 + l15;
+#pragma unroll
+        for (int r = 0; r < 4; ++r)
+          if (rows[r] < NPG)
+            bufA[(size_t)(nb + rows[r]) * HID + n2] = f2bf(acc[r] * sc[r]);
+      }
+    }
+  }
+  __syncthreads();
+
+  gather_stage(bufA + (size_t)nb * HID, csr, bufB + (size_t)nb * HID, &u,
+               s_hin, s_offs, s_sx, s_sq);
+
+  phi_stage<true>(bufB + (size_t)nb * HID, bufA + (size_t)nb * HID, Wt2, Rt1,
+                  r1b1, g1a, g1g, g1b, &u, sW, sR, s_hout, s_sx, s_sq,
+                  s_ps[0], s_hs[0]);
+
+  gather_stage(bufA + (size_t)nb * HID, csr, bufB + (size_t)nb * HID, &u,
+               s_hin, s_offs, s_sx, s_sq);
+
+  phi_stage<false>(bufB + (size_t)nb * HID, nullptr, nullptr, Rt2,
+                   r2b1, g2a, g2g, g2b, &u, sW, sR, s_hout, s_sx, s_sq,
+                   s_ps[1], s_hs[1]);
+
+  if (t < 64) {
+    float acc = r1b2[t];
 #pragma unroll 8
-  for (int k = 0; k < HID; ++k)
-    acc += (phi_sum[g * HID + k] * (1.0f / NPG)) * w2[k * RD + j];
-  const float r = leaky(acc);
-  out[g * 384 + roff + j] = leaky(r);
-  out[g * 384 + moff + j] = leaky(h_sum[g * HID + j] * (1.0f / NPG));
-  out[g * 384 + moff + 64 + j] = leaky(h_sum[g * HID + 64 + j] * (1.0f / NPG));
+    for (int k = 0; k < HID; ++k) acc += (s_ps[0][k] * (1.0f / NPG)) * r1w2[k * RD + t];
+    out[g * 384 + t] = leaky(leaky(acc));
+  } else if (t < 128) {
+    const int j = t - 64;
+    float acc = r2b2[j];
+#pragma unroll 8
+    for (int k = 0; k < HID; ++k) acc += (s_ps[1][k] * (1.0f / NPG)) * r2w2[k * RD + j];
+    out[g * 384 + 192 + j] = leaky(leaky(acc));
+  } else if (t < 256) {
+    const int j = t - 128;
+    out[g * 384 + 64 + j] = leaky(s_hs[0][j] * (1.0f / NPG));
+  } else if (t < 384) {
+    const int j = t - 256;
+    out[g * 384 + 256 + j] = leaky(s_hs[1][j] * (1.0f / NPG));
+  }
 }
 
 extern "C" void kernel_launch(void* const* d_in, const int* in_sizes, int n_in,
@@ -592,44 +524,18 @@
   float* out = (float*)d_out;
 
   char* wsb = (char*)d_ws;
-  float* ps1     = (float*)wsb;
-  float* hs1     = ps1 + NG * HID;
-  float* ps2     = hs1 + NG * HID;
-  float* hs2     = ps2 + NG * HID;
-  float* sx1     = hs2 + NG * HID;
-  float* sq1     = sx1 + NG * HID;
-  float* sx2     = sq1 + NG * HID;
-  float* sq2     = sx2 + NG * HID;
-  int*   cin     = (int*)(sq2 + NG * HID);
-  int*   cout_   = cin + NN;
-  int*   offs    = cout_ + NN;
-  unsigned* csr  = (unsigned*)(offs + NN);
-  u16*   Wt1     = (u16*)(csr + (size_t)NG * CSRG);
-  u16*   Wt2     = Wt1 + HID * FIN;
-  u16*   Rt1     = Wt2 + HID * HID;
-  u16*   Rt2     = Rt1 + HID * HID;
-  u16*   bufA    = Rt2 + HID * HID;
-  u16*   bufB    = bufA + (size_t)NN * HID;
-
-  hipMemsetAsync(d_ws, 0, (size_t)(8 * NG * HID) * sizeof(float), stream);
+  unsigned* csr = (unsigned*)wsb;
+  u16* Wt1  = (u16*)(csr + (size_t)NG * CSRG);
+  u16* Wt2  = Wt1 + HID * FIN;
+  u16* Rt1  = Wt2 + HID * HID;
+  u16* Rt2  = Rt1 + HID * HID;
+  u16* bufA = Rt2 + HID * HID;
+  u16* bufB = bufA + (size_t)NN * HID;
 
   wt_k<<<(FIN * HID + 3 * HID * HID) / 256, 256, 0, stream>>>(
       W1, W2, r1w1, r2w1, Wt1, Wt2, Rt1, Rt2);
-  build_k<<<8 * 13, 1024, 0, stream>>>(src, dst, ew, cin, cout_, offs, csr);
-
-  const int gemm_grid = 8 * 4 * 13;
-  const int gather_grid = 8 * 25 * 13;
-
-  gemm1_k<<<gemm_grid, 256, 0, stream>>>(node_feats, Wt1, cout_, bufA);
-  gather_k<<<gather_grid, 256, 0, stream>>>(bufA, csr, offs, cin, bufB, sx1, sq1);
-  phi_pool_k<<<gemm_grid, 256, 0, stream>>>(bufB, sx1, sq1, g1a, g1g, g1b,
-                                            Rt1, r1b1, ps1, hs1);
-  finalize_k<<<NG, 64, 0, stream>>>(ps1, hs1, r1w2, r1b2, out, 0, 64);
-
-  gemm_norm_k<<<gemm_grid, 256, 0, stream>>>(bufB, Wt2, sx1, sq1, g1a, g1g, g1b,
-                                             cout_, bufA);
-  gather_k<<<gather_grid, 256, 0, stream>>>(bufA, csr, offs, cin, bufB, sx2, sq2);
-  phi_pool_k<<<gemm_grid, 256, 0, stream>>>(bufB, sx2, sq2, g2a, g2g, g2b,
-                                            Rt2, r2b1, ps2, hs2);
-  finalize_k<<<NG, 64, 0, stream>>>(ps2, hs2, r2w2, r2b2, out, 192, 256);
-}
+  mega_k<<<NG, 1024, 0, stream>>>(node_feats, ew, src, dst, Wt1, Wt2, Rt1, Rt2,
+                                  g1a, g1g, g1b, g2a, g2g, g2b,
+                                  r1b1, r1w2, r1b2, r2b1, r2w2, r2b2,
+                                  csr, bufA, bufB, out);
+}
```

Result: slower. 484.3 us (+64.6%).
